# Performance work log

Hardware: AMD Instinct MI355X
Metric: run time of the kernel (lower is better)

Reference implementation:

```python
import jax, jax.numpy as jnp
import numpy as np

DT = 0.01  # module-level constant in the original source
H = 64


def _lstm_cell(x_in, h, c, W_ih, W_hh, b_ih, b_hh):
    # torch nn.LSTM gate order: i, f, g, o
    gates = x_in @ W_ih.T + h @ W_hh.T + (b_ih + b_hh)
    i, f, g, o = jnp.split(gates, 4, axis=-1)
    i = jax.nn.sigmoid(i)
    f = jax.nn.sigmoid(f)
    g = jnp.tanh(g)
    o = jax.nn.sigmoid(o)
    c_new = f * c + i * g
    h_new = o * jnp.tanh(c_new)
    return h_new, c_new


def setup_inputs() -> dict:
    key = jax.random.key(0)
    ks = jax.random.split(key, 12)
    B, x_size, s_size = 4096, 8, 8
    in_size = x_size + s_size
    sc = 1.0 / np.sqrt(H)

    def rn(k, shape, scale=1.0):
        return (jax.random.normal(k, shape, dtype=jnp.float32) * scale)

    return {
        "x": rn(ks[0], (B, 1, x_size)),
        "s0": rn(ks[1], (B, s_size)),
        "W_ih0": rn(ks[2], (4 * H, in_size), sc),
        "W_hh0": rn(ks[3], (4 * H, H), sc),
        "b_ih0": rn(ks[4], (4 * H,), sc),
        "b_hh0": rn(ks[5], (4 * H,), sc),
        "W_ih1": rn(ks[6], (4 * H, H), sc),
        "W_hh1": rn(ks[7], (4 * H, H), sc),
        "b_ih1": rn(ks[8], (4 * H,), sc),
        "b_hh1": rn(ks[9], (4 * H,), sc),
        "fc_W": rn(ks[10], (s_size, H), sc),
        "fc_b": rn(ks[11], (s_size,), sc),
        "num_steps": 1001,  # floor(max_time/dt)+1 with max_time=10.0
    }


def reference(x, s0, W_ih0, W_hh0, b_ih0, b_hh0, W_ih1, W_hh1, b_ih1, b_hh1,
              fc_W, fc_b, num_steps):
    B = x.shape[0]
    xin = x[:, 0, :]  # forward only ever reads x[:, 0:1] -> [B, x_size]
    h0 = jnp.zeros((B, H), x.dtype)

    def step(carry, _):
        s, h_a, c_a, h_b, c_b = carry
        combined = jnp.concatenate([xin, s], axis=-1)  # [B, x_size + s_size]
        h_a, c_a = _lstm_cell(combined, h_a, c_a, W_ih0, W_hh0, b_ih0, b_hh0)
        h_b, c_b = _lstm_cell(h_a, h_b, c_b, W_ih1, W_hh1, b_ih1, b_hh1)
        step_out = h_b @ fc_W.T + fc_b            # [B, s_size]
        s_new = s + step_out * DT                  # Euler integration
        return (s_new, h_a, c_a, h_b, c_b), (s_new, step_out)

    init = (s0, h0, h0, h0, h0)
    _, (outs, res) = jax.lax.scan(step, init, None, length=num_steps)
    outputs = jnp.transpose(outs, (1, 0, 2))       # [B, num_steps, s_size]
    res_step = jnp.transpose(res, (1, 0, 2))       # [B, num_steps, s_size]
    cal_times = jnp.arange(num_steps, dtype=jnp.float32) * DT
    return outputs, cal_times, res_step
```

## Files before the change

### kernel.cpp

```cpp
#include <hip/hip_runtime.h>

#define DTC 0.01f

typedef __attribute__((ext_vector_type(8))) short short8;
typedef __attribute__((ext_vector_type(4))) float floatx4;

#if __has_builtin(__builtin_amdgcn_exp2f)
#define EXP2F(x) __builtin_amdgcn_exp2f(x)
#else
#define EXP2F(x) exp2f(x)
#endif
#if __has_builtin(__builtin_amdgcn_rcpf)
#define RCPF(x) __builtin_amdgcn_rcpf(x)
#else
#define RCPF(x) (1.0f / (x))
#endif

__device__ __forceinline__ unsigned short f2bf(float f) {
    unsigned u = __float_as_uint(f);
    u += 0x7FFFu + ((u >> 16) & 1u);
    return (unsigned short)(u >> 16);
}
__device__ __forceinline__ float sigm(float x) {
    float e = EXP2F(-1.44269504089f * x);
    return RCPF(1.0f + e);
}
__device__ __forceinline__ float tanh_f(float x) {
    float e = EXP2F(2.88539008178f * x);
    return 1.0f - 2.0f * RCPF(e + 1.0f);
}

#define U0S 104
#define U1S 136

__global__ __launch_bounds__(256, 1) void lstm_mfma(
    const float* __restrict__ x,    const float* __restrict__ s0,
    const float* __restrict__ W_ih0,const float* __restrict__ W_hh0,
    const float* __restrict__ b_ih0,const float* __restrict__ b_hh0,
    const float* __restrict__ W_ih1,const float* __restrict__ W_hh1,
    const float* __restrict__ b_ih1,const float* __restrict__ b_hh1,
    const float* __restrict__ fc_W, const float* __restrict__ fc_b,
    const int* __restrict__ nsp,    float* __restrict__ out, int B)
{
    __shared__ unsigned short U0[16 * U0S];
    __shared__ unsigned short U1[16 * U1S];

    const int ns   = nsp[0];
    const int tid  = threadIdx.x;
    const int lane = tid & 63;
    const int wave = tid >> 6;
    const int il   = lane & 15;
    const int quad = lane >> 4;
    const int bb   = blockIdx.x * 16;

    float* cal = out + (size_t)B * ns * 8;
    float* res = cal + ns;

    if (blockIdx.x == 0)
        for (int t = tid; t < ns; t += 256) cal[t] = t * DTC;

    for (int i = tid; i < 16 * U0S; i += 256) U0[i] = 0;
    for (int i = tid; i < 16 * U1S; i += 256) U1[i] = 0;

    short8 B0[4][3], B1[4][4], BF[2];
    floatx4 bias0[4];
    float bias1[4];
    for (int j = 0; j < 4; ++j) {
        const int n = 64 * j + 16 * wave + il;
        for (int kk = 0; kk < 3; ++kk) {
            short8 f;
            #pragma unroll
            for (int jj = 0; jj < 8; ++jj) {
                int k = 32 * kk + 8 * quad + jj;
                float w;
                if (k < 64)      w = W_hh0[n * 64 + k];
                else if (k < 72) w = W_ih0[n * 16 + 8 + (k - 64)];
                else             w = 0.0f;
                f[jj] = (short)f2bf(w);
            }
            B0[j][kk] = f;
        }
        for (int kk = 0; kk < 4; ++kk) {
            short8 f;
            #pragma unroll
            for (int jj = 0; jj < 8; ++jj) {
                int k = 32 * kk + 8 * quad + jj;
                float w = (k < 64) ? W_ih1[n * 64 + k] : W_hh1[n * 64 + (k - 64)];
                f[jj] = (short)f2bf(w);
            }
            B1[j][kk] = f;
        }
        float bcol = b_ih0[n] + b_hh0[n];
        floatx4 bv;
        #pragma unroll
        for (int reg = 0; reg < 4; ++reg) {
            int m = 4 * quad + reg;
            float acc = bcol;
            for (int k = 0; k < 8; ++k)
                acc += x[(bb + m) * 8 + k] * W_ih0[n * 16 + k];
            bv[reg] = acc;
        }
        bias0[j] = bv;
        bias1[j] = b_ih1[n] + b_hh1[n];
    }
    for (int kk = 0; kk < 2; ++kk) {
        short8 f;
        #pragma unroll
        for (int jj = 0; jj < 8; ++jj) {
            int k = 32 * kk + 8 * quad + jj;
            float w = (il < 8) ? fc_W[il * 64 + k] : 0.0f;
            f[jj] = (short)f2bf(w);
        }
        BF[kk] = f;
    }
    const float fcb = (il < 8) ? fc_b[il] : 0.0f;

    float cA[4] = {0, 0, 0, 0}, cB[4] = {0, 0, 0, 0};
    float s_reg[4];
    #pragma unroll
    for (int reg = 0; reg < 4; ++reg) {
        int m = 4 * quad + reg;
        s_reg[reg] = (il < 8) ? s0[(bb + m) * 8 + il] : 0.0f;
    }
    if (wave == 0 && il < 8) {
        #pragma unroll
        for (int reg = 0; reg < 4; ++reg)
            U0[(4 * quad + reg) * U0S + 64 + il] = f2bf(s_reg[reg]);
    }
    __syncthreads();

    const int iidx = 16 * wave + il;

    #pragma unroll 1
    for (int t = 0; t < ns; ++t) {
        short8 a00 = *(const short8*)&U0[il * U0S + 0  + 8 * quad];
        short8 a01 = *(const short8*)&U0[il * U0S + 32 + 8 * quad];
        short8 a02 = *(const short8*)&U0[il * U0S + 64 + 8 * quad];
        short8 a12 = *(const short8*)&U1[il * U1S + 64 + 8 * quad];
        short8 a13 = *(const short8*)&U1[il * U1S + 96 + 8 * quad];
        __syncthreads();

        floatx4 g0[4];
        #pragma unroll
        for (int j = 0; j < 4; ++j) {
            floatx4 acc = bias0[j];
            acc = __builtin_amdgcn_mfma_f32_16x16x32_bf16(a00, B0[j][0], acc, 0, 0, 0);
            acc = __builtin_amdgcn_mfma_f32_16x16x32_bf16(a01, B0[j][1], acc, 0, 0, 0);
            acc = __builtin_amdgcn_mfma_f32_16x16x32_bf16(a02, B0[j][2], acc, 0, 0, 0);
            g0[j] = acc;
        }
        #pragma unroll
        for (int reg = 0; reg < 4; ++reg) {
            float ig = sigm(g0[0][reg]);
            float fg = sigm(g0[1][reg]);
            float gg = tanh_f(g0[2][reg]);
            float og = sigm(g0[3][reg]);
            float c  = fg * cA[reg] + ig * gg;
            cA[reg]  = c;
            unsigned short hb = f2bf(og * tanh_f(c));
            int m = 4 * quad + reg;
            U0[m * U0S + iidx] = hb;
            U1[m * U1S + iidx] = hb;
        }
        __syncthreads();

        short8 a10 = *(const short8*)&U1[il * U1S + 0  + 8 * quad];
        short8 a11 = *(const short8*)&U1[il * U1S + 32 + 8 * quad];
        floatx4 g1[4];
        #pragma unroll
        for (int j = 0; j < 4; ++j) {
            floatx4 acc = {bias1[j], bias1[j], bias1[j], bias1[j]};
            acc = __builtin_amdgcn_mfma_f32_16x16x32_bf16(a10, B1[j][0], acc, 0, 0, 0);
            acc = __builtin_amdgcn_mfma_f32_16x16x32_bf16(a11, B1[j][1], acc, 0, 0, 0);
            acc = __builtin_amdgcn_mfma_f32_16x16x32_bf16(a12, B1[j][2], acc, 0, 0, 0);
            acc = __builtin_amdgcn_mfma_f32_16x16x32_bf16(a13, B1[j][3], acc, 0, 0, 0);
            g1[j] = acc;
        }
        #pragma unroll
        for (int reg = 0; reg < 4; ++reg) {
            float ig = sigm(g1[0][reg]);
            float fg = sigm(g1[1][reg]);
            float gg = tanh_f(g1[2][reg]);
            float og = sigm(g1[3][reg]);
            float c  = fg * cB[reg] + ig * gg;
            cB[reg]  = c;
            int m = 4 * quad + reg;
            U1[m * U1S + 64 + iidx] = f2bf(og * tanh_f(c));
        }
        __syncthreads();

        short8 af0 = *(const short8*)&U1[il * U1S + 64 + 8 * quad];
        short8 af1 = *(const short8*)&U1[il * U1S + 96 + 8 * quad];
        floatx4 so = {fcb, fcb, fcb, fcb};
        so = __builtin_amdgcn_mfma_f32_16x16x32_bf16(af0, BF[0], so, 0, 0, 0);
        so = __builtin_amdgcn_mfma_f32_16x16x32_bf16(af1, BF[1], so, 0, 0, 0);

        #pragma unroll
        for (int reg = 0; reg < 4; ++reg) s_reg[reg] += so[reg] * DTC;

        if (wave == 0 && il < 8) {
            #pragma unroll
            for (int reg = 0; reg < 4; ++reg) {
                int m = 4 * quad + reg;
                U0[m * U0S + 64 + il] = f2bf(s_reg[reg]);
                size_t o = ((size_t)(bb + m) * ns + t) * 8 + il;
                out[o] = s_reg[reg];
                res[o] = so[reg];
            }
        }
        __syncthreads();
    }
}

extern "C" void kernel_launch(void* const* d_in, const int* in_sizes, int n_in,
                              void* d_out, int out_size, void* d_ws, size_t ws_size,
                              hipStream_t stream) {
    const float* x     = (const float*)d_in[0];
    const float* s0    = (const float*)d_in[1];
    const float* W_ih0 = (const float*)d_in[2];
    const float* W_hh0 = (const float*)d_in[3];
    const float* b_ih0 = (const float*)d_in[4];
    const float* b_hh0 = (const float*)d_in[5];
    const float* W_ih1 = (const float*)d_in[6];
    const float* W_hh1 = (const float*)d_in[7];
    const float* b_ih1 = (const float*)d_in[8];
    const float* b_hh1 = (const float*)d_in[9];
    const float* fc_W  = (const float*)d_in[10];
    const float* fc_b  = (const float*)d_in[11];
    const int*   nsp   = (const int*)d_in[12];
    (void)d_ws; (void)ws_size; (void)n_in; (void)out_size;
    int B = in_sizes[0] / 8;
    dim3 grid(B / 16), block(256);
    hipLaunchKernelGGL(lstm_mfma, grid, block, 0, stream,
        x, s0, W_ih0, W_hh0, b_ih0, b_hh0, W_ih1, W_hh1, b_ih1, b_hh1,
        fc_W, fc_b, nsp, (float*)d_out, B);
}
```

Baseline: 1.545 ms.

## Fold FC and Euler update into layer-0 gates, cut barriers per step

```diff
diff --git a/kernel.cpp b/kernel.cpp
--- a/kernel.cpp
+++ b/kernel.cpp
@@ -1,6 +1,8 @@
 #include <hip/hip_runtime.h>
 
 #define DTC 0.01f
+#define LAM  2.88539008178f
+#define L2E  1.44269504089f
 
 typedef __attribute__((ext_vector_type(8))) short short8;
 typedef __attribute__((ext_vector_type(4))) float floatx4;
@@ -21,17 +23,17 @@
     u += 0x7FFFu + ((u >> 16) & 1u);
     return (unsigned short)(u >> 16);
 }
-__device__ __forceinline__ float sigm(float x) {
-    float e = EXP2F(-1.44269504089f * x);
-    return RCPF(1.0f + e);
-}
-__device__ __forceinline__ float tanh_f(float x) {
-    float e = EXP2F(2.88539008178f * x);
-    return 1.0f - 2.0f * RCPF(e + 1.0f);
-}
-
-#define U0S 104
+__device__ __forceinline__ float rcp1p(float y) {
+    return RCPF(1.0f + EXP2F(y));
+}
+__device__ __forceinline__ void wg_barrier() {
+    asm volatile("s_waitcnt lgkmcnt(0)" ::: "memory");
+    __builtin_amdgcn_s_barrier();
+}
+
 #define U1S 136
+
+#define MFMA(a, b, c) __builtin_amdgcn_mfma_f32_16x16x32_bf16((a), (b), (c), 0, 0, 0)
 
 __global__ __launch_bounds__(256, 1) void lstm_mfma(
     const float* __restrict__ x,    const float* __restrict__ s0,
@@ -42,8 +44,7 @@
     const float* __restrict__ fc_W, const float* __restrict__ fc_b,
     const int* __restrict__ nsp,    float* __restrict__ out, int B)
 {
-    __shared__ unsigned short U0[16 * U0S];
-    __shared__ unsigned short U1[16 * U1S];
+    __shared__ __align__(16) unsigned short U1[16 * U1S];
 
     const int ns   = nsp[0];
     const int tid  = threadIdx.x;
@@ -59,50 +60,75 @@
     if (blockIdx.x == 0)
         for (int t = tid; t < ns; t += 256) cal[t] = t * DTC;
 
-    for (int i = tid; i < 16 * U0S; i += 256) U0[i] = 0;
     for (int i = tid; i < 16 * U1S; i += 256) U1[i] = 0;
 
-    short8 B0[4][3], B1[4][4], BF[2];
-    floatx4 bias0[4];
-    float bias1[4];
+    short8 B0[4][2], B1[4][4], M2f[4][2], BF[2];
+    floatx4 gs[4], bias1v[4];
+    float gd[4];
+
     for (int j = 0; j < 4; ++j) {
+        const float gam = (j == 2) ? LAM : -L2E;
         const int n = 64 * j + 16 * wave + il;
-        for (int kk = 0; kk < 3; ++kk) {
+        float ws[8];
+        #pragma unroll
+        for (int p = 0; p < 8; ++p) ws[p] = W_ih0[n * 16 + 8 + p];
+
+        #pragma unroll
+        for (int kk = 0; kk < 2; ++kk) {
             short8 f;
             #pragma unroll
             for (int jj = 0; jj < 8; ++jj) {
                 int k = 32 * kk + 8 * quad + jj;
-                float w;
-                if (k < 64)      w = W_hh0[n * 64 + k];
-                else if (k < 72) w = W_ih0[n * 16 + 8 + (k - 64)];
-                else             w = 0.0f;
-                f[jj] = (short)f2bf(w);
+                f[jj] = (short)f2bf(gam * W_hh0[n * 64 + k]);
             }
             B0[j][kk] = f;
         }
+        #pragma unroll
         for (int kk = 0; kk < 4; ++kk) {
             short8 f;
             #pragma unroll
             for (int jj = 0; jj < 8; ++jj) {
                 int k = 32 * kk + 8 * quad + jj;
                 float w = (k < 64) ? W_ih1[n * 64 + k] : W_hh1[n * 64 + (k - 64)];
-                f[jj] = (short)f2bf(w);
+                f[jj] = (short)f2bf(gam * w);
             }
             B1[j][kk] = f;
         }
+        #pragma unroll
+        for (int kk = 0; kk < 2; ++kk) {
+            short8 f;
+            #pragma unroll
+            for (int jj = 0; jj < 8; ++jj) {
+                int k = 32 * kk + 8 * quad + jj;
+                float acc = 0.0f;
+                #pragma unroll
+                for (int p = 0; p < 8; ++p) acc += ws[p] * fc_W[p * 64 + k];
+                f[jj] = (short)f2bf(gam * DTC * acc);
+            }
+            M2f[j][kk] = f;
+        }
+        float accb = 0.0f;
+        #pragma unroll
+        for (int p = 0; p < 8; ++p) accb += ws[p] * fc_b[p];
+        gd[j] = gam * DTC * accb;
+
         float bcol = b_ih0[n] + b_hh0[n];
-        floatx4 bv;
+        floatx4 gv;
         #pragma unroll
         for (int reg = 0; reg < 4; ++reg) {
             int m = 4 * quad + reg;
             float acc = bcol;
-            for (int k = 0; k < 8; ++k)
-                acc += x[(bb + m) * 8 + k] * W_ih0[n * 16 + k];
-            bv[reg] = acc;
-        }
-        bias0[j] = bv;
-        bias1[j] = b_ih1[n] + b_hh1[n];
-    }
+            #pragma unroll
+            for (int k = 0; k < 8; ++k) acc += x[(bb + m) * 8 + k] * W_ih0[n * 16 + k];
+            #pragma unroll
+            for (int p = 0; p < 8; ++p) acc += ws[p] * s0[(bb + m) * 8 + p];
+            gv[reg] = gam * acc - gd[j];
+        }
+        gs[j] = gv;
+        float b1 = gam * (b_ih1[n] + b_hh1[n]);
+        bias1v[j] = (floatx4){b1, b1, b1, b1};
+    }
+    #pragma unroll
     for (int kk = 0; kk < 2; ++kk) {
         short8 f;
         #pragma unroll
@@ -122,93 +148,118 @@
         int m = 4 * quad + reg;
         s_reg[reg] = (il < 8) ? s0[(bb + m) * 8 + il] : 0.0f;
     }
-    if (wave == 0 && il < 8) {
-        #pragma unroll
-        for (int reg = 0; reg < 4; ++reg)
-            U0[(4 * quad + reg) * U0S + 64 + il] = f2bf(s_reg[reg]);
-    }
-    __syncthreads();
-
+
+    short8 a10 = {0, 0, 0, 0, 0, 0, 0, 0};
+    short8 a11 = {0, 0, 0, 0, 0, 0, 0, 0};
     const int iidx = 16 * wave + il;
+    wg_barrier();
 
     #pragma unroll 1
     for (int t = 0; t < ns; ++t) {
-        short8 a00 = *(const short8*)&U0[il * U0S + 0  + 8 * quad];
-        short8 a01 = *(const short8*)&U0[il * U0S + 32 + 8 * quad];
-        short8 a02 = *(const short8*)&U0[il * U0S + 64 + 8 * quad];
         short8 a12 = *(const short8*)&U1[il * U1S + 64 + 8 * quad];
         short8 a13 = *(const short8*)&U1[il * U1S + 96 + 8 * quad];
-        __syncthreads();
 
         floatx4 g0[4];
         #pragma unroll
         for (int j = 0; j < 4; ++j) {
-            floatx4 acc = bias0[j];
-            acc = __builtin_amdgcn_mfma_f32_16x16x32_bf16(a00, B0[j][0], acc, 0, 0, 0);
-            acc = __builtin_amdgcn_mfma_f32_16x16x32_bf16(a01, B0[j][1], acc, 0, 0, 0);
-            acc = __builtin_amdgcn_mfma_f32_16x16x32_bf16(a02, B0[j][2], acc, 0, 0, 0);
-            g0[j] = acc;
-        }
-        #pragma unroll
-        for (int reg = 0; reg < 4; ++reg) {
-            float ig = sigm(g0[0][reg]);
-            float fg = sigm(g0[1][reg]);
-            float gg = tanh_f(g0[2][reg]);
-            float og = sigm(g0[3][reg]);
-            float c  = fg * cA[reg] + ig * gg;
+            floatx4 z = {0.f, 0.f, 0.f, 0.f};
+            z = MFMA(a10, B0[j][0], z);
+            z = MFMA(a11, B0[j][1], z);
+            g0[j] = z;
+        }
+        #pragma unroll
+        for (int j = 0; j < 4; ++j) {
+            floatx4 z = gs[j];
+            z = MFMA(a12, M2f[j][0], z);
+            z = MFMA(a13, M2f[j][1], z);
+            #pragma unroll
+            for (int reg = 0; reg < 4; ++reg) z[reg] += gd[j];
+            gs[j] = z;
+        }
+        floatx4 p1[4];
+        #pragma unroll
+        for (int j = 0; j < 4; ++j) {
+            floatx4 z = bias1v[j];
+            z = MFMA(a12, B1[j][2], z);
+            z = MFMA(a13, B1[j][3], z);
+            p1[j] = z;
+        }
+        #pragma unroll
+        for (int reg = 0; reg < 4; ++reg) {
+            float iv = rcp1p(g0[0][reg] + gs[0][reg]);
+            float fv = rcp1p(g0[1][reg] + gs[1][reg]);
+            float gr = rcp1p(g0[2][reg] + gs[2][reg]);
+            float gl = __builtin_fmaf(gr, -2.0f * LAM, LAM);
+            float ov = rcp1p(g0[3][reg] + gs[3][reg]);
+            float c  = __builtin_fmaf(fv, cA[reg], iv * gl);
             cA[reg]  = c;
-            unsigned short hb = f2bf(og * tanh_f(c));
-            int m = 4 * quad + reg;
-            U0[m * U0S + iidx] = hb;
-            U1[m * U1S + iidx] = hb;
-        }
-        __syncthreads();
-
-        short8 a10 = *(const short8*)&U1[il * U1S + 0  + 8 * quad];
-        short8 a11 = *(const short8*)&U1[il * U1S + 32 + 8 * quad];
+            float r2 = rcp1p(c);
+            float u  = ov * r2;
+            float h  = __builtin_fmaf(-2.0f, u, ov);
+            U1[(4 * quad + reg) * U1S + iidx] = f2bf(h);
+        }
+        wg_barrier();
+
+        a10 = *(const short8*)&U1[il * U1S + 0  + 8 * quad];
+        a11 = *(const short8*)&U1[il * U1S + 32 + 8 * quad];
+
+        if (t && wave == 0) {
+            floatx4 so = {fcb, fcb, fcb, fcb};
+            so = MFMA(a12, BF[0], so);
+            so = MFMA(a13, BF[1], so);
+            #pragma unroll
+            for (int reg = 0; reg < 4; ++reg) {
+                s_reg[reg] += so[reg] * DTC;
+                if (il < 8) {
+                    int m = 4 * quad + reg;
+                    size_t o = ((size_t)(bb + m) * ns + (t - 1)) * 8 + il;
+                    out[o] = s_reg[reg];
+                    res[o] = so[reg];
+                }
+            }
+        }
+
         floatx4 g1[4];
         #pragma unroll
         for (int j = 0; j < 4; ++j) {
-            floatx4 acc = {bias1[j], bias1[j], bias1[j], bias1[j]};
-            acc = __builtin_amdgcn_mfma_f32_16x16x32_bf16(a10, B1[j][0], acc, 0, 0, 0);
-            acc = __builtin_amdgcn_mfma_f32_16x16x32_bf16(a11, B1[j][1], acc, 0, 0, 0);
-            acc = __builtin_amdgcn_mfma_f32_16x16x32_bf16(a12, B1[j][2], acc, 0, 0, 0);
-            acc = __builtin_amdgcn_mfma_f32_16x16x32_bf16(a13, B1[j][3], acc, 0, 0, 0);
-            g1[j] = acc;
-        }
-        #pragma unroll
-        for (int reg = 0; reg < 4; ++reg) {
-            float ig = sigm(g1[0][reg]);
-            float fg = sigm(g1[1][reg]);
-            float gg = tanh_f(g1[2][reg]);
-            float og = sigm(g1[3][reg]);
-            float c  = fg * cB[reg] + ig * gg;
+            floatx4 z = p1[j];
+            z = MFMA(a10, B1[j][0], z);
+            z = MFMA(a11, B1[j][1], z);
+            g1[j] = z;
+        }
+        #pragma unroll
+        for (int reg = 0; reg < 4; ++reg) {
+            float iv = rcp1p(g1[0][reg]);
+            float fv = rcp1p(g1[1][reg]);
+            float gr = rcp1p(g1[2][reg]);
+            float gl = __builtin_fmaf(gr, -2.0f * LAM, LAM);
+            float ov = rcp1p(g1[3][reg]);
+            float c  = __builtin_fmaf(fv, cB[reg], iv * gl);
             cB[reg]  = c;
-            int m = 4 * quad + reg;
-            U1[m * U1S + 64 + iidx] = f2bf(og * tanh_f(c));
-        }
-        __syncthreads();
-
-        short8 af0 = *(const short8*)&U1[il * U1S + 64 + 8 * quad];
-        short8 af1 = *(const short8*)&U1[il * U1S + 96 + 8 * quad];
+            float r2 = rcp1p(c);
+            float u  = ov * r2;
+            float h  = __builtin_fmaf(-2.0f, u, ov);
+            U1[(4 * quad + reg) * U1S + 64 + iidx] = f2bf(h);
+        }
+        wg_barrier();
+    }
+
+    if (wave == 0) {
+        short8 a12 = *(const short8*)&U1[il * U1S + 64 + 8 * quad];
+        short8 a13 = *(const short8*)&U1[il * U1S + 96 + 8 * quad];
         floatx4 so = {fcb, fcb, fcb, fcb};
-        so = __builtin_amdgcn_mfma_f32_16x16x32_bf16(af0, BF[0], so, 0, 0, 0);
-        so = __builtin_amdgcn_mfma_f32_16x16x32_bf16(af1, BF[1], so, 0, 0, 0);
-
-        #pragma unroll
-        for (int reg = 0; reg < 4; ++reg) s_reg[reg] += so[reg] * DTC;
-
-        if (wave == 0 && il < 8) {
-            #pragma unroll
-            for (int reg = 0; reg < 4; ++reg) {
+        so = MFMA(a12, BF[0], so);
+        so = MFMA(a13, BF[1], so);
+        #pragma unroll
+        for (int reg = 0; reg < 4; ++reg) {
+            s_reg[reg] += so[reg] * DTC;
+            if (il < 8) {
                 int m = 4 * quad + reg;
-                U0[m * U0S + 64 + il] = f2bf(s_reg[reg]);
-                size_t o = ((size_t)(bb + m) * ns + t) * 8 + il;
+                size_t o = ((size_t)(bb + m) * ns + (ns - 1)) * 8 + il;
                 out[o] = s_reg[reg];
                 res[o] = so[reg];
             }
         }
-        __syncthreads();
     }
 }
 
```

After: 1.399 ms. 1.1x faster.
